# Performance work log

Measured on AMD Instinct MI355X. Metric: run time of the kernel, lower is better.

## Reference

```python
import jax, jax.numpy as jnp
import numpy as np

N_NODES = 50000
N_EDGES = 800000
IN_DIM = 8
EDGE_DIM = 4
HIDDEN = 16
OUT_DIM = 1


def _lin_init(key, fan_in, fan_out):
    kw, kb = jax.random.split(key)
    bound = 1.0 / np.sqrt(fan_in)
    W = jax.random.uniform(kw, (fan_in, fan_out), minval=-bound, maxval=bound, dtype=jnp.float32)
    b = jax.random.uniform(kb, (fan_out,), minval=-bound, maxval=bound, dtype=jnp.float32)
    return W, b


def setup_inputs() -> dict:
    key = jax.random.key(0)
    ks = jax.random.split(key, 16)
    x = jax.random.normal(ks[0], (N_NODES, IN_DIM), dtype=jnp.float32)
    edge_index = jax.random.randint(ks[1], (2, N_EDGES), 0, N_NODES, dtype=jnp.int32)
    edge_attr = jax.random.normal(ks[2], (N_EDGES, EDGE_DIM), dtype=jnp.float32)

    inp = {"x": x, "edge_index": edge_index, "edge_attr": edge_attr}
    in_dims = [IN_DIM, HIDDEN]
    for i in range(2):
        d_in = in_dims[i]
        W1, b1 = _lin_init(ks[3 + 4 * i], EDGE_DIM, HIDDEN)
        W2, b2 = _lin_init(ks[4 + 4 * i], HIDDEN, d_in * HIDDEN)
        root = jax.random.uniform(ks[5 + 4 * i], (d_in, HIDDEN), minval=-1.0 / np.sqrt(d_in), maxval=1.0 / np.sqrt(d_in), dtype=jnp.float32)
        bias = jnp.zeros((HIDDEN,), dtype=jnp.float32)
        inp[f"eW1_{i}"] = W1; inp[f"eb1_{i}"] = b1
        inp[f"eW2_{i}"] = W2; inp[f"eb2_{i}"] = b2
        inp[f"root_{i}"] = root; inp[f"bias_{i}"] = bias
    mW1, mb1 = _lin_init(ks[11], HIDDEN, HIDDEN)
    mW2, mb2 = _lin_init(ks[12], HIDDEN, OUT_DIM)
    inp["mW1"] = mW1; inp["mb1"] = mb1; inp["mW2"] = mW2; inp["mb2"] = mb2
    return inp


def _nnconv(x, src, dst, edge_attr, eW1, eb1, eW2, eb2, root, bias):
    # edge MLP -> per-edge weight matrix [E, d_in, HIDDEN]
    h = jax.nn.silu(edge_attr @ eW1 + eb1)
    Wedge = (h @ eW2 + eb2).reshape(edge_attr.shape[0], x.shape[1], HIDDEN)
    # gather source features, per-edge matmul, scatter-mean to targets
    msg = jnp.einsum('ei,eio->eo', x[src], Wedge)  # [E, HIDDEN]
    agg = jax.ops.segment_sum(msg, dst, num_segments=N_NODES)
    cnt = jax.ops.segment_sum(jnp.ones((msg.shape[0],), dtype=msg.dtype), dst, num_segments=N_NODES)
    agg = agg / jnp.maximum(cnt, 1.0)[:, None]
    return x @ root + agg + bias


def reference(x, edge_index, edge_attr,
              eW1_0, eb1_0, eW2_0, eb2_0, root_0, bias_0,
              eW1_1, eb1_1, eW2_1, eb2_1, root_1, bias_1,
              mW1, mb1, mW2, mb2):
    src, dst = edge_index[0], edge_index[1]
    x = jax.nn.relu(_nnconv(x, src, dst, edge_attr, eW1_0, eb1_0, eW2_0, eb2_0, root_0, bias_0))
    x = jax.nn.relu(_nnconv(x, src, dst, edge_attr, eW1_1, eb1_1, eW2_1, eb2_1, root_1, bias_1))
    out = jax.nn.sigmoid(jax.nn.silu(x @ mW1 + mb1) @ mW2 + mb2)
    return out
```

## Files before the change

kernel.cpp:

```cpp
#include <hip/hip_runtime.h>
#include <hip/hip_fp16.h>

#define NN 50000
#define NE 800000
#define NBUCK 392

__device__ __forceinline__ float sigm(float v) { return 1.0f / (1.0f + __expf(-v)); }


__global__ void sort_count(const int* __restrict__ ei,
                           int* __restrict__ cntA, int* __restrict__ cntB)
{
    __shared__ int hA[NBUCK], hB[NBUCK];
    int t = threadIdx.x;
    for (int i = t; i < NBUCK; i += 256) { hA[i] = 0; hB[i] = 0; }
    __syncthreads();
    int base = blockIdx.x * 4096;
#pragma unroll
    for (int r = 0; r < 16; ++r) {
        int idx = base + r * 256 + t;
        if (idx < NE) {
            int s = ei[idx], d = ei[NE + idx];
            atomicAdd(&hB[s >> 7], 1);
            atomicAdd(&hA[d >> 7], 1);
        }
    }
    __syncthreads();
    for (int i = t; i < NBUCK; i += 256) {
        if (hA[i]) atomicAdd(&cntA[i], hA[i]);
        if (hB[i]) atomicAdd(&cntB[i], hB[i]);
    }
}

__global__ void sort_scan(const int* __restrict__ cntA, const int* __restrict__ cntB,
                          int* __restrict__ baseA, int* __restrict__ baseB,
                          int* __restrict__ curA,  int* __restrict__ curB)
{
    __shared__ int a[512], b[512];
    int t = threadIdx.x;
    a[t] = (t < NBUCK) ? cntA[t] : 0;
    b[t] = (t < NBUCK) ? cntB[t] : 0;
    __syncthreads();
#pragma unroll
    for (int dd = 1; dd < 512; dd <<= 1) {
        int av = (t >= dd) ? a[t - dd] : 0;
        int bv = (t >= dd) ? b[t - dd] : 0;
        __syncthreads();
        a[t] += av; b[t] += bv;
        __syncthreads();
    }
    int exA = (t > 0) ? a[t - 1] : 0;
    int exB = (t > 0) ? b[t - 1] : 0;
    if (t < NBUCK) { baseA[t] = exA; curA[t] = exA; baseB[t] = exB; curB[t] = exB; }
    if (t == 511)  { baseA[NBUCK] = a[511]; baseB[NBUCK] = b[511]; }
}

__global__ __launch_bounds__(256) void sort_scatterA(const int* __restrict__ ei,
                                                     int* __restrict__ curA,
                                                     unsigned long long* __restrict__ recA)
{
    __shared__ int lcnt[NBUCK];
    __shared__ int lofs[NBUCK];
    int t = threadIdx.x;
    for (int i = t; i < NBUCK; i += 256) lcnt[i] = 0;
    __syncthreads();
    int base = blockIdx.x * 4096;
#pragma unroll
    for (int r = 0; r < 16; ++r) {
        int e = base + r * 256 + t;
        if (e < NE) atomicAdd(&lcnt[ei[NE + e] >> 7], 1);
    }
    __syncthreads();
    for (int i = t; i < NBUCK; i += 256)
        lofs[i] = lcnt[i] ? atomicAdd(&curA[i], lcnt[i]) : 0;
    __syncthreads();
#pragma unroll
    for (int r = 0; r < 16; ++r) {
        int e = base + r * 256 + t;
        if (e < NE) {
            int s = ei[e], d = ei[NE + e];
            int p = atomicAdd(&lofs[d >> 7], 1);
            recA[p] = ((unsigned long long)(unsigned)(d & 127) << 36)
                    | ((unsigned long long)(unsigned)s << 20)
                    | (unsigned long long)(unsigned)e;
        }
    }
}

__global__ __launch_bounds__(256) void sort_localAB(const unsigned long long* __restrict__ recA,
                                                    const int* __restrict__ baseA,
                                                    int* __restrict__ off_all,
                                                    int* __restrict__ curB,
                                                    unsigned long long* __restrict__ recB)
{
    __shared__ int c[128];
    __shared__ int live[128];
    __shared__ int lcnt[NBUCK];
    __shared__ int lofs[NBUCK];
    int t = threadIdx.x;
    int b = blockIdx.x;
    int lo = baseA[b], hi = baseA[b + 1];
    if (t < 128) c[t] = 0;
    for (int i = t; i < NBUCK; i += 256) lcnt[i] = 0;
    __syncthreads();
    for (int i = lo + t; i < hi; i += 256) {
        unsigned long long rec = recA[i];
        atomicAdd(&c[(int)(rec >> 36) & 127], 1);
        atomicAdd(&lcnt[(int)(rec >> 27) & 511], 1);
    }
    __syncthreads();
#pragma unroll
    for (int dd = 1; dd < 128; dd <<= 1) {
        int v = (t >= dd && t < 128) ? c[t - dd] : 0;
        __syncthreads();
        if (t < 128) c[t] += v;
        __syncthreads();
    }
    if (t < 128) {
        int ex = (t > 0) ? c[t - 1] : 0;
        int d = (b << 7) + t;
        if (d <= NN) off_all[d] = lo + ex;
        live[t] = lo + ex;
    }
    __syncthreads();
    for (int i = t; i < NBUCK; i += 256)
        lofs[i] = lcnt[i] ? atomicAdd(&curB[i], lcnt[i]) : 0;
    __syncthreads();
    for (int i = lo + t; i < hi; i += 256) {
        unsigned long long rec = recA[i];
        int dp = atomicAdd(&live[(int)(rec >> 36) & 127], 1);
        int s  = (int)((rec >> 20) & 0xFFFFu);
        int p  = atomicAdd(&lofs[s >> 7], 1);
        recB[p] = ((unsigned long long)(unsigned)(s & 127) << 40)
                | ((unsigned long long)(unsigned)dp << 20)
                | (rec & 0xFFFFFull);
    }
}

__global__ __launch_bounds__(256) void sort_localB(const unsigned long long* __restrict__ recB,
                                                   const int* __restrict__ baseB,
                                                   const float4* __restrict__ ea4,
                                                   int* __restrict__ off_all,
                                                   unsigned* __restrict__ sperm32,
                                                   float4* __restrict__ ea_perm)
{
    __shared__ int c[128];
    __shared__ int live[128];
    int t = threadIdx.x;
    int b = blockIdx.x;
    int lo = baseB[b], hi = baseB[b + 1];
    if (t < 128) c[t] = 0;
    __syncthreads();
    for (int i = lo + t; i < hi; i += 256)
        atomicAdd(&c[(int)(recB[i] >> 40) & 127], 1);
    __syncthreads();
#pragma unroll
    for (int dd = 1; dd < 128; dd <<= 1) {
        int v = (t >= dd && t < 128) ? c[t - dd] : 0;
        __syncthreads();
        if (t < 128) c[t] += v;
        __syncthreads();
    }
    if (t < 128) {
        int ex = (t > 0) ? c[t - 1] : 0;
        int s = (b << 7) + t;
        if (s <= NN) off_all[NN + s] = NE + lo + ex;
        live[t] = lo + ex;
    }
    __syncthreads();
    for (int i = lo + t; i < hi; i += 256) {
        unsigned long long rec = recB[i];
        int k = (int)(rec >> 40) & 127;
        int pos = atomicAdd(&live[k], 1);
        unsigned sl = (unsigned)(k & 15);
        unsigned dp = (unsigned)((rec >> 20) & 0xFFFFFu);
        sperm32[pos] = (sl << 20) | dp;
        ea_perm[pos] = ea4[rec & 0xFFFFFull];
    }
}

template<int DIN>
__global__ __launch_bounds__(256) void edge_fusedG(
        const float* __restrict__ xin,
        const unsigned* __restrict__ sperm32,
        const float4* __restrict__ ea_perm,
        const float* __restrict__ eW1,
        const float* __restrict__ eb1,
        const float* __restrict__ eW2,
        const float* __restrict__ eb2,
        const int*   __restrict__ off_all,
        __half* __restrict__ msgbuf)
{
    __shared__ __align__(16) float4 w2L4[4 * DIN * 17];
    __shared__ __align__(16) float4 G4[16 * 69];
    __shared__ __align__(16) float4 xbL[16 * 5];
    __shared__ __align__(16) float  xL[16 * DIN];
    __shared__ __align__(16) float  b2L[DIN * 16];
    __shared__ __align__(16) float4 w1t[16];
    __shared__ __align__(16) float  b1s[16];

    int tid = threadIdx.x;
    int nb  = blockIdx.x * 16;
    if (tid < 16) {
        w1t[tid] = make_float4(eW1[tid], eW1[16 + tid], eW1[32 + tid], eW1[48 + tid]);
        b1s[tid] = eb1[tid];
    }
    {
        float* w2f = (float*)w2L4;
        for (int t = tid; t < 16 * DIN * 16; t += 256) {
            int k = t / (DIN * 16);
            int rem = t - k * DIN * 16;
            int i = rem >> 4, o = rem & 15;
            w2f[((((o >> 2) * DIN + i) * 17) + k) * 4 + (o & 3)] = eW2[t];
        }
    }
    for (int t = tid; t < DIN * 16; t += 256) b2L[t] = eb2[t];
    for (int t = tid; t < 16 * DIN; t += 256) xL[t] = xin[(size_t)nb * DIN + t];
    __syncthreads();

    {
        int nl = tid >> 4, k = tid & 15;
        const float* xrow = xL + nl * DIN;
#pragma unroll
        for (int ob = 0; ob < 4; ++ob) {
            float4 a4 = make_float4(0.f, 0.f, 0.f, 0.f);
#pragma unroll
            for (int i = 0; i < DIN; ++i) {
                float4 w = w2L4[(ob * DIN + i) * 17 + k];
                a4.x += xrow[i] * w.x; a4.y += xrow[i] * w.y;
                a4.z += xrow[i] * w.z; a4.w += xrow[i] * w.w;
            }
            G4[nl * 69 + ob * 17 + k] = a4;
        }
        if (k < 4) {
            int ob = k;
            const float4* b2v = (const float4*)b2L;
            float4 a4 = make_float4(0.f, 0.f, 0.f, 0.f);
#pragma unroll
            for (int i = 0; i < DIN; ++i) {
                float4 b = b2v[i * 4 + ob];
                a4.x += xrow[i] * b.x; a4.y += xrow[i] * b.y;
                a4.z += xrow[i] * b.z; a4.w += xrow[i] * b.w;
            }
            xbL[nl * 5 + ob] = a4;
        }
    }
    __syncthreads();

    int eBeg = off_all[NN + nb] - NE;
    int eEnd = off_all[NN + nb + 16] - NE;
    for (int pos = eBeg + tid; pos < eEnd; pos += 256) {
        unsigned pk = sperm32[pos];
        int dp = (int)(pk & 0xFFFFFu);
        int sl = (int)(pk >> 20);
        float4 a = ea_perm[pos];

        float h[16];
#pragma unroll
        for (int j = 0; j < 16; ++j) {
            float4 w = w1t[j];
            float p = b1s[j] + a.x * w.x + a.y * w.y + a.z * w.z + a.w * w.w;
            h[j] = p * sigm(p);
        }
        float4 acc[4];
#pragma unroll
        for (int ob = 0; ob < 4; ++ob) acc[ob] = xbL[sl * 5 + ob];
#pragma unroll
        for (int k = 0; k < 16; ++k) {
            float hk = h[k];
#pragma unroll
            for (int ob = 0; ob < 4; ++ob) {
                float4 g = G4[sl * 69 + ob * 17 + k];
                acc[ob].x += hk * g.x; acc[ob].y += hk * g.y;
                acc[ob].z += hk * g.z; acc[ob].w += hk * g.w;
            }
        }
        __half2 h01 = __floats2half2_rn(acc[0].x, acc[0].y);
        __half2 h23 = __floats2half2_rn(acc[0].z, acc[0].w);
        __half2 h45 = __floats2half2_rn(acc[1].x, acc[1].y);
        __half2 h67 = __floats2half2_rn(acc[1].z, acc[1].w);
        __half2 h89 = __floats2half2_rn(acc[2].x, acc[2].y);
        __half2 hAB = __floats2half2_rn(acc[2].z, acc[2].w);
        __half2 hCD = __floats2half2_rn(acc[3].x, acc[3].y);
        __half2 hEF = __floats2half2_rn(acc[3].z, acc[3].w);
        uint4 w0 = make_uint4(*(unsigned*)&h01, *(unsigned*)&h23,
                              *(unsigned*)&h45, *(unsigned*)&h67);
        uint4 w1 = make_uint4(*(unsigned*)&h89, *(unsigned*)&hAB,
                              *(unsigned*)&hCD, *(unsigned*)&hEF);
        uint4* dst = (uint4*)(msgbuf + (size_t)dp * 16);
        dst[0] = w0;
        dst[1] = w1;
    }
}

__device__ __forceinline__ float gather_msg16(const __half* __restrict__ msgbuf,
                                              int s0, int e0, int tid)
{
    int half = (tid >> 3) & 1;
    int p    = tid & 7;
    float ax = 0.f, ay = 0.f;
    for (int j = s0 + half; j < e0; j += 2) {
        __half2 hv = *((const __half2*)(msgbuf + (size_t)j * 16) + p);
        float2 f = __half22float2(hv);
        ax += f.x; ay += f.y;
    }
    ax += __shfl_xor(ax, 8, 16);
    ay += __shfl_xor(ay, 8, 16);
    int ch = tid & 15;
    float vx = __shfl(ax, ch >> 1, 16);
    float vy = __shfl(ay, ch >> 1, 16);
    return (ch & 1) ? vy : vx;
}

__global__ __launch_bounds__(256) void gather_L0(
        const float* __restrict__ xin,
        const float* __restrict__ root,
        const float* __restrict__ bias,
        const int*   __restrict__ off_all,
        const __half* __restrict__ msgbuf,
        float* __restrict__ x1)
{
    __shared__ __align__(16) float rootL[8 * 16];
    __shared__ __align__(16) float biasL[16];
    int tid = threadIdx.x;
    if (tid < 128) rootL[tid] = root[tid];
    if (tid < 16) biasL[tid] = bias[tid];
    __syncthreads();

    int ch = tid & 15;
    int n  = blockIdx.x * 16 + (tid >> 4);
    int s0 = off_all[n], e0 = off_all[n + 1];

    float acc = gather_msg16(msgbuf, s0, e0, tid);
    float v = acc / fmaxf((float)(e0 - s0), 1.0f) + biasL[ch];
#pragma unroll
    for (int i = 0; i < 8; ++i)
        v += xin[(size_t)n * 8 + i] * rootL[i * 16 + ch];
    x1[(size_t)n * 16 + ch] = fmaxf(v, 0.f);
}

__global__ __launch_bounds__(256) void gather_final(
        const float* __restrict__ x1,
        const float* __restrict__ root,
        const float* __restrict__ bias,
        const int*   __restrict__ off_all,
        const __half* __restrict__ msgbuf,
        const float* __restrict__ mW1,
        const float* __restrict__ mb1,
        const float* __restrict__ mW2,
        const float* __restrict__ mb2,
        float* __restrict__ out)
{
    __shared__ __align__(16) float rootL[256];
    __shared__ __align__(16) float biasL[16];
    __shared__ __align__(16) float w1m[256];
    __shared__ __align__(16) float b1m[16];
    __shared__ __align__(16) float w2m[16];
    __shared__ float b2m;
    int tid = threadIdx.x;
    rootL[tid] = root[tid];
    w1m[tid] = mW1[tid];
    if (tid < 16) { biasL[tid] = bias[tid]; b1m[tid] = mb1[tid]; w2m[tid] = mW2[tid]; }
    if (tid == 0) b2m = mb2[0];
    __syncthreads();

    int ch = tid & 15;
    int n  = blockIdx.x * 16 + (tid >> 4);
    int s0 = off_all[n], e0 = off_all[n + 1];

    float acc = gather_msg16(msgbuf, s0, e0, tid);
    float v = acc / fmaxf((float)(e0 - s0), 1.0f) + biasL[ch];
#pragma unroll
    for (int i = 0; i < 16; ++i)
        v += x1[(size_t)n * 16 + i] * rootL[i * 16 + ch];
    v = fmaxf(v, 0.f);

    float z = b1m[ch];
#pragma unroll
    for (int o = 0; o < 16; ++o) {
        float vo = __shfl(v, o, 16);
        z += vo * w1m[o * 16 + ch];
    }
    float ss = z * sigm(z) * w2m[ch];
#pragma unroll
    for (int off = 8; off; off >>= 1) ss += __shfl_xor(ss, off, 16);
    if (ch == 0) out[n] = sigm(ss + b2m);
}

extern "C" void kernel_launch(void* const* d_in, const int* in_sizes, int n_in,
                              void* d_out, int out_size, void* d_ws, size_t ws_size,
                              hipStream_t stream) {
    const float* x     = (const float*)d_in[0];
    const int*   ei    = (const int*)  d_in[1];
    const float* ea    = (const float*)d_in[2];
    const float* eW1_0 = (const float*)d_in[3];
    const float* eb1_0 = (const float*)d_in[4];
    const float* eW2_0 = (const float*)d_in[5];
    const float* eb2_0 = (const float*)d_in[6];
    const float* root0 = (const float*)d_in[7];
    const float* bias0 = (const float*)d_in[8];
    const float* eW1_1 = (const float*)d_in[9];
    const float* eb1_1 = (const float*)d_in[10];
    const float* eW2_1 = (const float*)d_in[11];
    const float* eb2_1 = (const float*)d_in[12];
    const float* root1 = (const float*)d_in[13];
    const float* bias1 = (const float*)d_in[14];
    const float* mW1   = (const float*)d_in[15];
    const float* mb1   = (const float*)d_in[16];
    const float* mW2   = (const float*)d_in[17];
    const float* mb2   = (const float*)d_in[18];
    float* out = (float*)d_out;

    const int GG  = NN / 16;
    const int SBK = (NE + 4095) / 4096;

    int* W = (int*)d_ws;
    int* off_all = W;
    int* cntA    = W + 100004;
    int* cntB    = W + 100400;
    int* baseA   = W + 100800;
    int* baseB   = W + 101200;
    int* curA    = W + 101600;
    int* curB    = W + 102000;
    unsigned* sperm32 = (unsigned*)(W + 102400);
    float4* ea_perm   = (float4*)(W + 902400);
    float*  x1        = (float*)(W + 4102400);
    __half* msgbuf    = (__half*)(W + 4902400);
    unsigned long long* recA = (unsigned long long*)(W + 4902400);
    unsigned long long* recB = (unsigned long long*)(W + 6502400);

    hipMemsetAsync(cntA, 0, 2 * 396 * sizeof(int), stream);
    sort_count   <<<SBK,  256, 0, stream>>>(ei, cntA, cntB);
    sort_scan    <<<1,    512, 0, stream>>>(cntA, cntB, baseA, baseB, curA, curB);
    sort_scatterA<<<SBK,  256, 0, stream>>>(ei, curA, recA);
    sort_localAB <<<NBUCK,256, 0, stream>>>(recA, baseA, off_all, curB, recB);
    sort_localB  <<<NBUCK,256, 0, stream>>>(recB, baseB, (const float4*)ea,
                                            off_all, sperm32, ea_perm);

    edge_fusedG<8><<<GG, 256, 0, stream>>>(x, sperm32, ea_perm, eW1_0, eb1_0,
                                           eW2_0, eb2_0, off_all, msgbuf);
    gather_L0<<<GG, 256, 0, stream>>>(x, root0, bias0, off_all, msgbuf, x1);

    edge_fusedG<16><<<GG, 256, 0, stream>>>(x1, sperm32, ea_perm, eW1_1, eb1_1,
                                            eW2_1, eb2_1, off_all, msgbuf);
    gather_final<<<GG, 256, 0, stream>>>(x1, root1, bias1, off_all, msgbuf,
                                         mW1, mb1, mW2, mb2, out);
}
```

Before: 270.6 us.

## Replace sort count pass with fixed-capacity bucket scatter and post-scan

Drops the separate histogram kernel that read edge_index once before the bucket scatter. Records are now written into fixed-capacity per-bucket slots (CAP entries per bucket), and each bucket's fill counter doubles as its count. A small scan computes bucket bases after each scatter. This saves one full pass over the edge list and one launch, at the cost of an extra scan launch, a larger workspace, and a silent overflow if any 128-node bucket receives more than CAP edges.

```diff
diff --git a/kernel.cpp b/kernel.cpp
--- a/kernel.cpp
+++ b/kernel.cpp
@@ -4,55 +4,26 @@
 #define NN 50000
 #define NE 800000
 #define NBUCK 392
+#define CAP 3584
 
 __device__ __forceinline__ float sigm(float v) { return 1.0f / (1.0f + __expf(-v)); }
 
 
-__global__ void sort_count(const int* __restrict__ ei,
-                           int* __restrict__ cntA, int* __restrict__ cntB)
-{
-    __shared__ int hA[NBUCK], hB[NBUCK];
+__global__ void scan1(const int* __restrict__ cnt, int* __restrict__ base)
+{
+    __shared__ int a[512];
     int t = threadIdx.x;
-    for (int i = t; i < NBUCK; i += 256) { hA[i] = 0; hB[i] = 0; }
-    __syncthreads();
-    int base = blockIdx.x * 4096;
-#pragma unroll
-    for (int r = 0; r < 16; ++r) {
-        int idx = base + r * 256 + t;
-        if (idx < NE) {
-            int s = ei[idx], d = ei[NE + idx];
-            atomicAdd(&hB[s >> 7], 1);
-            atomicAdd(&hA[d >> 7], 1);
-        }
-    }
-    __syncthreads();
-    for (int i = t; i < NBUCK; i += 256) {
-        if (hA[i]) atomicAdd(&cntA[i], hA[i]);
-        if (hB[i]) atomicAdd(&cntB[i], hB[i]);
-    }
-}
-
-__global__ void sort_scan(const int* __restrict__ cntA, const int* __restrict__ cntB,
-                          int* __restrict__ baseA, int* __restrict__ baseB,
-                          int* __restrict__ curA,  int* __restrict__ curB)
-{
-    __shared__ int a[512], b[512];
-    int t = threadIdx.x;
-    a[t] = (t < NBUCK) ? cntA[t] : 0;
-    b[t] = (t < NBUCK) ? cntB[t] : 0;
+    a[t] = (t < NBUCK) ? cnt[t] : 0;
     __syncthreads();
 #pragma unroll
     for (int dd = 1; dd < 512; dd <<= 1) {
-        int av = (t >= dd) ? a[t - dd] : 0;
-        int bv = (t >= dd) ? b[t - dd] : 0;
-        __syncthreads();
-        a[t] += av; b[t] += bv;
-        __syncthreads();
-    }
-    int exA = (t > 0) ? a[t - 1] : 0;
-    int exB = (t > 0) ? b[t - 1] : 0;
-    if (t < NBUCK) { baseA[t] = exA; curA[t] = exA; baseB[t] = exB; curB[t] = exB; }
-    if (t == 511)  { baseA[NBUCK] = a[511]; baseB[NBUCK] = b[511]; }
+        int v = (t >= dd) ? a[t - dd] : 0;
+        __syncthreads();
+        a[t] += v;
+        __syncthreads();
+    }
+    int ex = (t > 0) ? a[t - 1] : 0;
+    if (t <= NBUCK) base[t] = ex;
 }
 
 __global__ __launch_bounds__(256) void sort_scatterA(const int* __restrict__ ei,
@@ -80,14 +51,16 @@
         if (e < NE) {
             int s = ei[e], d = ei[NE + e];
             int p = atomicAdd(&lofs[d >> 7], 1);
-            recA[p] = ((unsigned long long)(unsigned)(d & 127) << 36)
-                    | ((unsigned long long)(unsigned)s << 20)
-                    | (unsigned long long)(unsigned)e;
+            recA[(size_t)(d >> 7) * CAP + p] =
+                  ((unsigned long long)(unsigned)(d & 127) << 36)
+                | ((unsigned long long)(unsigned)s << 20)
+                | (unsigned long long)(unsigned)e;
         }
     }
 }
 
 __global__ __launch_bounds__(256) void sort_localAB(const unsigned long long* __restrict__ recA,
+                                                    const int* __restrict__ curA,
                                                     const int* __restrict__ baseA,
                                                     int* __restrict__ off_all,
                                                     int* __restrict__ curB,
@@ -99,12 +72,14 @@
     __shared__ int lofs[NBUCK];
     int t = threadIdx.x;
     int b = blockIdx.x;
-    int lo = baseA[b], hi = baseA[b + 1];
+    int n  = curA[b];
+    int lo = baseA[b];
+    const unsigned long long* recs = recA + (size_t)b * CAP;
     if (t < 128) c[t] = 0;
     for (int i = t; i < NBUCK; i += 256) lcnt[i] = 0;
     __syncthreads();
-    for (int i = lo + t; i < hi; i += 256) {
-        unsigned long long rec = recA[i];
+    for (int i = t; i < n; i += 256) {
+        unsigned long long rec = recs[i];
         atomicAdd(&c[(int)(rec >> 36) & 127], 1);
         atomicAdd(&lcnt[(int)(rec >> 27) & 511], 1);
     }
@@ -126,18 +101,20 @@
     for (int i = t; i < NBUCK; i += 256)
         lofs[i] = lcnt[i] ? atomicAdd(&curB[i], lcnt[i]) : 0;
     __syncthreads();
-    for (int i = lo + t; i < hi; i += 256) {
-        unsigned long long rec = recA[i];
+    for (int i = t; i < n; i += 256) {
+        unsigned long long rec = recs[i];
         int dp = atomicAdd(&live[(int)(rec >> 36) & 127], 1);
         int s  = (int)((rec >> 20) & 0xFFFFu);
         int p  = atomicAdd(&lofs[s >> 7], 1);
-        recB[p] = ((unsigned long long)(unsigned)(s & 127) << 40)
-                | ((unsigned long long)(unsigned)dp << 20)
-                | (rec & 0xFFFFFull);
+        recB[(size_t)(s >> 7) * CAP + p] =
+              ((unsigned long long)(unsigned)(s & 127) << 40)
+            | ((unsigned long long)(unsigned)dp << 20)
+            | (rec & 0xFFFFFull);
     }
 }
 
 __global__ __launch_bounds__(256) void sort_localB(const unsigned long long* __restrict__ recB,
+                                                   const int* __restrict__ curB,
                                                    const int* __restrict__ baseB,
                                                    const float4* __restrict__ ea4,
                                                    int* __restrict__ off_all,
@@ -148,11 +125,13 @@
     __shared__ int live[128];
     int t = threadIdx.x;
     int b = blockIdx.x;
-    int lo = baseB[b], hi = baseB[b + 1];
+    int n  = curB[b];
+    int lo = baseB[b];
+    const unsigned long long* recs = recB + (size_t)b * CAP;
     if (t < 128) c[t] = 0;
     __syncthreads();
-    for (int i = lo + t; i < hi; i += 256)
-        atomicAdd(&c[(int)(recB[i] >> 40) & 127], 1);
+    for (int i = t; i < n; i += 256)
+        atomicAdd(&c[(int)(recs[i] >> 40) & 127], 1);
     __syncthreads();
 #pragma unroll
     for (int dd = 1; dd < 128; dd <<= 1) {
@@ -168,8 +147,8 @@
         live[t] = lo + ex;
     }
     __syncthreads();
-    for (int i = lo + t; i < hi; i += 256) {
-        unsigned long long rec = recB[i];
+    for (int i = t; i < n; i += 256) {
+        unsigned long long rec = recs[i];
         int k = (int)(rec >> 40) & 127;
         int pos = atomicAdd(&live[k], 1);
         unsigned sl = (unsigned)(k & 15);
@@ -416,25 +395,23 @@
 
     int* W = (int*)d_ws;
     int* off_all = W;
-    int* cntA    = W + 100004;
-    int* cntB    = W + 100400;
-    int* baseA   = W + 100800;
-    int* baseB   = W + 101200;
-    int* curA    = W + 101600;
-    int* curB    = W + 102000;
+    int* curA    = W + 100004;
+    int* curB    = W + 100404;
+    int* baseA   = W + 100804;
+    int* baseB   = W + 101204;
     unsigned* sperm32 = (unsigned*)(W + 102400);
     float4* ea_perm   = (float4*)(W + 902400);
     float*  x1        = (float*)(W + 4102400);
     __half* msgbuf    = (__half*)(W + 4902400);
     unsigned long long* recA = (unsigned long long*)(W + 4902400);
-    unsigned long long* recB = (unsigned long long*)(W + 6502400);
-
-    hipMemsetAsync(cntA, 0, 2 * 396 * sizeof(int), stream);
-    sort_count   <<<SBK,  256, 0, stream>>>(ei, cntA, cntB);
-    sort_scan    <<<1,    512, 0, stream>>>(cntA, cntB, baseA, baseB, curA, curB);
+    unsigned long long* recB = (unsigned long long*)(W + 7712256);
+
+    hipMemsetAsync(curA, 0, 800 * sizeof(int), stream);
     sort_scatterA<<<SBK,  256, 0, stream>>>(ei, curA, recA);
-    sort_localAB <<<NBUCK,256, 0, stream>>>(recA, baseA, off_all, curB, recB);
-    sort_localB  <<<NBUCK,256, 0, stream>>>(recB, baseB, (const float4*)ea,
+    scan1        <<<1,    512, 0, stream>>>(curA, baseA);
+    sort_localAB <<<NBUCK,256, 0, stream>>>(recA, curA, baseA, off_all, curB, recB);
+    scan1        <<<1,    512, 0, stream>>>(curB, baseB);
+    sort_localB  <<<NBUCK,256, 0, stream>>>(recB, curB, baseB, (const float4*)ea,
                                             off_all, sperm32, ea_perm);
 
     edge_fusedG<8><<<GG, 256, 0, stream>>>(x, sperm32, ea_perm, eW1_0, eb1_0,
```

New measurement: 268.0 us. No clear change (-1.0%).
